# Kernel tuning notes

Hardware: AMD Instinct MI355X
Metric: run time of the kernel (lower is better)

The kernel has to match this reference:

```python
import jax, jax.numpy as jnp
import numpy as np

N_NODES = 100000
N_EDGES = 1600000
DIMS = [512, 200, 175, 125, 75, 50]


def setup_inputs() -> dict:
    key = jax.random.key(0)
    ks = jax.random.split(key, 12)
    inp = {
        "x": jax.random.normal(ks[0], (N_NODES, DIMS[0]), dtype=jnp.float32),
        "edge_index": jax.random.randint(ks[1], (2, N_EDGES), 0, N_NODES, dtype=jnp.int32),
    }
    for i in range(5):
        fan_in, fan_out = DIMS[i], DIMS[i + 1]
        scale = 1.0 / np.sqrt(fan_in)
        inp[f"W{i+1}"] = jax.random.uniform(ks[2 + 2 * i], (fan_in, fan_out), minval=-scale, maxval=scale, dtype=jnp.float32)
        inp[f"b{i+1}"] = jnp.zeros((fan_out,), dtype=jnp.float32)
    return inp


def _gcn_norm(edge_index, n_nodes):
    # add self loops, then symmetric normalization D^-1/2 (A+I) D^-1/2
    loop = jnp.arange(n_nodes, dtype=edge_index.dtype)
    src = jnp.concatenate([edge_index[0], loop])
    dst = jnp.concatenate([edge_index[1], loop])
    deg = jax.ops.segment_sum(jnp.ones_like(dst, dtype=jnp.float32), dst, num_segments=n_nodes)
    dinv = jnp.where(deg > 0, jax.lax.rsqrt(deg), 0.0)
    norm = dinv[src] * dinv[dst]  # [E+N]
    return src, dst, norm


def _gcn_layer(x, W, b, src, dst, norm, n_nodes):
    h = x @ W                                   # [N, out] dense GEMM
    msg = h[src] * norm[:, None]                # gather + scale  [E+N, out]
    agg = jax.ops.segment_sum(msg, dst, num_segments=n_nodes)  # scatter-add
    return agg + b


def reference(x, edge_index, W1, b1, W2, b2, W3, b3, W4, b4, W5, b5):
    n = x.shape[0]
    src, dst, norm = _gcn_norm(edge_index, n)
    h = jax.nn.relu(_gcn_layer(x, W1, b1, src, dst, norm, n))
    h = jax.nn.relu(_gcn_layer(h, W2, b2, src, dst, norm, n))
    h = jax.nn.relu(_gcn_layer(h, W3, b3, src, dst, norm, n))
    h = jax.nn.relu(_gcn_layer(h, W4, b4, src, dst, norm, n))
    return _gcn_layer(h, W5, b5, src, dst, norm, n)
```

## Files before the change

### kernel.cpp

```cpp
#include <hip/hip_runtime.h>
#include <hip/hip_bf16.h>


typedef float f32x4 __attribute__((ext_vector_type(4)));
typedef short bf16x8 __attribute__((ext_vector_type(8)));

static const int GDIMS[6] = {512, 200, 175, 125, 75, 50};
static const int GPAD[6]  = {512, 224, 192, 128, 96, 64};


__global__ void zero_kernel(int* __restrict__ p, int n) {
    int i = blockIdx.x * blockDim.x + threadIdx.x;
    for (; i < n; i += gridDim.x * blockDim.x) p[i] = 0;
}

__global__ void hist_kernel(const int* __restrict__ dst, int E, int* __restrict__ deg) {
    int i = blockIdx.x * blockDim.x + threadIdx.x;
    for (; i < E; i += gridDim.x * blockDim.x) atomicAdd(&deg[dst[i]], 1);
}

__global__ __launch_bounds__(1024) void scan_kernel(const int* __restrict__ deg,
                                                    int* __restrict__ rowptr, int N) {
    __shared__ int sums[1024];
    int t = threadIdx.x;
    int chunk = (N + 1023) >> 10;
    int lo = t * chunk;
    int hi = lo + chunk; if (hi > N) hi = N;
    if (lo > N) lo = N;
    int s = 0;
    for (int i = lo; i < hi; ++i) s += deg[i];
    sums[t] = s;
    __syncthreads();
    for (int off = 1; off < 1024; off <<= 1) {
        int v = (t >= off) ? sums[t - off] : 0;
        __syncthreads();
        sums[t] += v;
        __syncthreads();
    }
    int run = (t > 0) ? sums[t - 1] : 0;
    for (int i = lo; i < hi; ++i) { rowptr[i] = run; run += deg[i]; }
    if (t == 1023) rowptr[N] = run;
}

__global__ void dinv_kernel(const int* __restrict__ deg, float* __restrict__ dinv, int N) {
    int i = blockIdx.x * blockDim.x + threadIdx.x;
    for (; i < N; i += gridDim.x * blockDim.x)
        dinv[i] = rsqrtf((float)(deg[i] + 1));
}

__global__ void copy_kernel(const int* __restrict__ a, int* __restrict__ b, int n) {
    int i = blockIdx.x * blockDim.x + threadIdx.x;
    for (; i < n; i += gridDim.x * blockDim.x) b[i] = a[i];
}

__global__ void scatter_kernel(const int* __restrict__ src, const int* __restrict__ dst,
                               int E, int* __restrict__ cursor, int* __restrict__ csrc) {
    int i = blockIdx.x * blockDim.x + threadIdx.x;
    for (; i < E; i += gridDim.x * blockDim.x) {
        int d = dst[i];
        int pos = atomicAdd(&cursor[d], 1);
        csrc[pos] = src[i];
    }
}


__global__ void wsplit_kernel(const float* __restrict__ W, int K, int Nout,
                              int Kp, ushort* __restrict__ Whi, ushort* __restrict__ Wlo) {
    int k = blockIdx.x * blockDim.x + threadIdx.x;
    int n = blockIdx.y;
    if (k >= Kp) return;
    float v = (k < K && n < Nout) ? W[(size_t)k * Nout + n] : 0.f;
    __bf16 h = (__bf16)v;
    ushort hb = __builtin_bit_cast(ushort, h);
    float hf = __builtin_bit_cast(float, (unsigned)hb << 16);
    __bf16 l = (__bf16)(v - hf);
    Whi[(size_t)n * Kp + k] = hb;
    Wlo[(size_t)n * Kp + k] = __builtin_bit_cast(ushort, l);
}


__device__ inline f32x4 mfma16(bf16x8 a, bf16x8 b, f32x4 c) {
    return __builtin_amdgcn_mfma_f32_16x16x32_bf16(a, b, c, 0, 0, 0);
}

__device__ inline void split8(f32x4 a0, f32x4 a1, bf16x8& hi, bf16x8& lo) {
    float af[8] = {a0[0], a0[1], a0[2], a0[3], a1[0], a1[1], a1[2], a1[3]};
#pragma unroll
    for (int e = 0; e < 8; ++e) {
        __bf16 h = (__bf16)af[e];
        ushort hb = __builtin_bit_cast(ushort, h);
        float hf = __builtin_bit_cast(float, (unsigned)hb << 16);
        __bf16 l = (__bf16)(af[e] - hf);
        hi[e] = (short)hb;
        lo[e] = __builtin_bit_cast(short, l);
    }
}

template<int WM, int WN>
__global__ __launch_bounds__(WM * WN * 64) void gemm_t(
    const float* __restrict__ A, int lda, int Arows,
    const ushort* __restrict__ Bhi, const ushort* __restrict__ Blo, int Kp,
    const float* __restrict__ dinv, int N,
    float* __restrict__ C, int ldc)
{
    constexpr int BM = WM * 64;
    constexpr int T = WM * WN * 64;
    constexpr int SROW = BM + 2;
    __shared__ ushort Ah[4 * SROW * 8];
    __shared__ ushort Al[4 * SROW * 8];

    const int tid = threadIdx.x;
    const int lane = tid & 63;
    const int wave = tid >> 6;
    const int wm = (WM == 1) ? 0 : (wave % WM);
    const int wn = (WM == 1) ? wave : (wave / WM);
    const int m0 = blockIdx.x * BM;
    const int kg = lane >> 4;
    const int l16 = lane & 15;

    const ushort* bp[4];
#pragma unroll
    for (int fn = 0; fn < 4; ++fn) {
        int n = wn * 64 + fn * 16 + l16;
        bp[fn] = Bhi + (size_t)n * Kp + kg * 8;
    }
    const size_t lo_off = (size_t)(Blo - Bhi);

    f32x4 acc[4][4];
#pragma unroll
    for (int i = 0; i < 4; ++i)
#pragma unroll
        for (int j = 0; j < 4; ++j) acc[i][j] = (f32x4)0.f;

    for (int k0 = 0; k0 < Kp; k0 += 32) {
        for (int j = tid; j < BM * 4; j += T) {
            int row = j >> 2, jk = j & 3;
            int gr = m0 + row; if (gr > Arows - 1) gr = Arows - 1;
            const float* ap = A + (size_t)gr * lda + k0 + jk * 8;
            f32x4 a0 = *(const f32x4*)ap;
            f32x4 a1 = *(const f32x4*)(ap + 4);
            bf16x8 hi, lo;
            split8(a0, a1, hi, lo);
            int idx = (jk * SROW + row) * 8;
            *(bf16x8*)&Ah[idx] = hi;
            *(bf16x8*)&Al[idx] = lo;
        }
        __syncthreads();

        bf16x8 bh[4], bl[4], ah[4], al[4];
#pragma unroll
        for (int fn = 0; fn < 4; ++fn) {
            bh[fn] = *(const bf16x8*)(bp[fn] + k0);
            bl[fn] = *(const bf16x8*)(bp[fn] + lo_off + k0);
        }
#pragma unroll
        for (int fm = 0; fm < 4; ++fm) {
            int idx = (kg * SROW + wm * 64 + fm * 16 + l16) * 8;
            ah[fm] = *(const bf16x8*)&Ah[idx];
            al[fm] = *(const bf16x8*)&Al[idx];
        }
#pragma unroll
        for (int fm = 0; fm < 4; ++fm)
#pragma unroll
            for (int fn = 0; fn < 4; ++fn) {
                acc[fm][fn] = mfma16(ah[fm], bh[fn], acc[fm][fn]);
                acc[fm][fn] = mfma16(ah[fm], bl[fn], acc[fm][fn]);
                acc[fm][fn] = mfma16(al[fm], bh[fn], acc[fm][fn]);
            }
        __syncthreads();
    }

    float dv[4][4];
#pragma unroll
    for (int fm = 0; fm < 4; ++fm)
#pragma unroll
        for (int r = 0; r < 4; ++r) {
            int row = m0 + wm * 64 + fm * 16 + kg * 4 + r;
            dv[fm][r] = (row < N) ? dinv[row] : 0.f;
        }
#pragma unroll
    for (int fm = 0; fm < 4; ++fm)
#pragma unroll
        for (int fn = 0; fn < 4; ++fn) {
            int col = wn * 64 + fn * 16 + l16;
            if (col < ldc) {
#pragma unroll
                for (int r = 0; r < 4; ++r) {
                    int row = m0 + wm * 64 + fm * 16 + kg * 4 + r;
                    C[(size_t)row * ldc + col] = acc[fm][fn][r] * dv[fm][r];
                }
            }
        }
}


template<int L>
__global__ __launch_bounds__(256) void agg_t(
    const float* __restrict__ g, int ldg, int nd4,
    const int* __restrict__ rowptr, const int* __restrict__ csrc,
    const float* __restrict__ dinv, const float* __restrict__ bias,
    int D, int N, float* __restrict__ out, int ldo, int relu, int fin)
{
    int node = blockIdx.x * (256 / L) + threadIdx.x / L;
    if (node >= N) return;
    int f4 = threadIdx.x & (L - 1);
    if (f4 >= nd4) return;

    const f32x4* g4 = (const f32x4*)g;
    int ld4 = ldg >> 2;
    f32x4 a0 = g4[(size_t)node * ld4 + f4];
    f32x4 a1 = (f32x4)0.f, a2 = (f32x4)0.f, a3 = (f32x4)0.f;
    int beg = rowptr[node], end = rowptr[node + 1];
    int j = beg;
    for (; j + 3 < end; j += 4) {
        int s0 = csrc[j], s1 = csrc[j + 1], s2 = csrc[j + 2], s3 = csrc[j + 3];
        a0 += g4[(size_t)s0 * ld4 + f4];
        a1 += g4[(size_t)s1 * ld4 + f4];
        a2 += g4[(size_t)s2 * ld4 + f4];
        a3 += g4[(size_t)s3 * ld4 + f4];
    }
    for (; j < end; ++j) a0 += g4[(size_t)csrc[j] * ld4 + f4];

    f32x4 s = (a0 + a1) + (a2 + a3);
    float di = dinv[node];
    if (fin) {
#pragma unroll
        for (int e = 0; e < 4; ++e) {
            int f = f4 * 4 + e;
            if (f < D) out[(size_t)node * ldo + f] = fmaf(di, s[e], bias[f]);
        }
    } else {
        f32x4 v;
#pragma unroll
        for (int e = 0; e < 4; ++e) {
            int f = f4 * 4 + e;
            float val = (f < D) ? fmaf(di, s[e], bias[f]) : 0.f;
            if (relu) val = fmaxf(val, 0.f);
            v[e] = val;
        }
        *(f32x4*)(out + (size_t)node * ldo + f4 * 4) = v;
    }
}


extern "C" void kernel_launch(void* const* d_in, const int* in_sizes, int n_in,
                              void* d_out, int out_size, void* d_ws, size_t ws_size,
                              hipStream_t stream) {
    const float* x = (const float*)d_in[0];
    const int* ei = (const int*)d_in[1];
    int E = in_sizes[1] / 2;
    int N = in_sizes[0] / GDIMS[0];
    int Mp = ((N + 255) / 256) * 256;
    const int* src = ei;
    const int* dst = ei + E;

    const float* W[5];
    const float* bia[5];
    for (int i = 0; i < 5; ++i) {
        W[i] = (const float*)d_in[2 + 2 * i];
        bia[i] = (const float*)d_in[3 + 2 * i];
    }

    char* ws = (char*)d_ws;
    size_t off = 0;
    auto alloc = [&](size_t bytes) -> void* {
        void* p = ws + off;
        off += (bytes + 255) & ~(size_t)255;
        return p;
    };
    int* deg = (int*)alloc((size_t)N * 4);
    int* rowptr = (int*)alloc((size_t)(N + 1) * 4);
    int* cursor = (int*)alloc((size_t)N * 4);
    float* dinv = (float*)alloc((size_t)N * 4);
    int* csrc = (int*)alloc((size_t)E * 4);
    float* buf0 = (float*)alloc((size_t)Mp * 224 * 4);
    float* buf1 = (float*)alloc((size_t)Mp * 224 * 4);
    ushort* Whi[5];
    ushort* Wlo[5];
    int NB[5];
    for (int l = 0; l < 5; ++l) {
        int Kp = GPAD[l];
        NB[l] = ((GPAD[l + 1] + 63) / 64) * 64;
        if (l == 0) NB[l] = 256;
        Whi[l] = (ushort*)alloc((size_t)NB[l] * Kp * 2);
        Wlo[l] = (ushort*)alloc((size_t)NB[l] * Kp * 2);
    }
    (void)ws_size;

    zero_kernel<<<1024, 256, 0, stream>>>(deg, N);
    hist_kernel<<<2048, 256, 0, stream>>>(dst, E, deg);
    scan_kernel<<<1, 1024, 0, stream>>>(deg, rowptr, N);
    dinv_kernel<<<512, 256, 0, stream>>>(deg, dinv, N);
    copy_kernel<<<512, 256, 0, stream>>>(rowptr, cursor, N);
    scatter_kernel<<<2048, 256, 0, stream>>>(src, dst, E, cursor, csrc);

    for (int l = 0; l < 5; ++l) {
        int Kp = GPAD[l];
        dim3 gw((Kp + 255) / 256, NB[l]);
        wsplit_kernel<<<gw, 256, 0, stream>>>(W[l], GDIMS[l], GDIMS[l + 1], Kp,
                                              Whi[l], Wlo[l]);
    }

    for (int l = 0; l < 5; ++l) {
        int Kp = GPAD[l];
        int Pout = GPAD[l + 1];
        int D = GDIMS[l + 1];
        const float* Ain = (l == 0) ? x : buf1;
        int lda = GPAD[l];

        if (l == 0) {
            gemm_t<1, 4><<<Mp / 64, 256, 0, stream>>>(Ain, lda, N, Whi[l], Wlo[l], Kp,
                                                      dinv, N, buf0, Pout);
        } else if (l == 1) {
            gemm_t<1, 3><<<Mp / 64, 192, 0, stream>>>(Ain, lda, N, Whi[l], Wlo[l], Kp,
                                                      dinv, N, buf0, Pout);
        } else if (l == 2 || l == 3) {
            gemm_t<2, 2><<<Mp / 128, 256, 0, stream>>>(Ain, lda, N, Whi[l], Wlo[l], Kp,
                                                       dinv, N, buf0, Pout);
        } else {
            gemm_t<4, 1><<<Mp / 256, 256, 0, stream>>>(Ain, lda, N, Whi[l], Wlo[l], Kp,
                                                       dinv, N, buf0, Pout);
        }

        int nd4 = (D + 3) / 4;
        float* outp = (l == 4) ? (float*)d_out : buf1;
        int ldo = (l == 4) ? D : Pout;
        int relu = (l < 4) ? 1 : 0;
        int fin = (l == 4) ? 1 : 0;
        if (l <= 1) {
            int npb = 256 / 64;
            agg_t<64><<<(N + npb - 1) / npb, 256, 0, stream>>>(buf0, Pout, nd4, rowptr,
                                                               csrc, dinv, bia[l], D, N,
                                                               outp, ldo, relu, fin);
        } else if (l <= 3) {
            int npb = 256 / 32;
            agg_t<32><<<(N + npb - 1) / npb, 256, 0, stream>>>(buf0, Pout, nd4, rowptr,
                                                               csrc, dinv, bia[l], D, N,
                                                               outp, ldo, relu, fin);
        } else {
            int npb = 256 / 16;
            agg_t<16><<<(N + npb - 1) / npb, 256, 0, stream>>>(buf0, Pout, nd4, rowptr,
                                                               csrc, dinv, bia[l], D, N,
                                                               outp, ldo, relu, fin);
        }
    }
    (void)out_size; (void)n_in;
}
```

Baseline: 1.294 ms.

## Emit bf16 hi/lo activations from aggregation and add direct-load bf16 GEMM

The aggregation kernel now writes the next layer's input already split into bf16 hi/lo planes, so layers 2-5 use a new GEMM that loads pre-split operands straight from global memory with no LDS staging or per-tile conversion. Aggregation threads are packed densely per node (only the needed float4 lanes), which removes idle lanes. The gather loop is unrolled to 8 independent accumulators. This trades the LDS-based GEMM for uncached direct global loads and adds an extra write of the split activations.

```diff
diff --git a/kernel.cpp b/kernel.cpp
--- a/kernel.cpp
+++ b/kernel.cpp
@@ -4,6 +4,7 @@
 
 typedef float f32x4 __attribute__((ext_vector_type(4)));
 typedef short bf16x8 __attribute__((ext_vector_type(8)));
+typedef ushort u16x4 __attribute__((ext_vector_type(4)));
 
 static const int GDIMS[6] = {512, 200, 175, 125, 75, 50};
 static const int GPAD[6]  = {512, 224, 192, 128, 96, 64};
@@ -96,8 +97,9 @@
     }
 }
 
+
 template<int WM, int WN>
-__global__ __launch_bounds__(WM * WN * 64) void gemm_t(
+__global__ __launch_bounds__(WM * WN * 64) void gemm_f32(
     const float* __restrict__ A, int lda, int Arows,
     const ushort* __restrict__ Bhi, const ushort* __restrict__ Blo, int Kp,
     const float* __restrict__ dinv, int N,
@@ -170,14 +172,6 @@
         __syncthreads();
     }
 
-    float dv[4][4];
-#pragma unroll
-    for (int fm = 0; fm < 4; ++fm)
-#pragma unroll
-        for (int r = 0; r < 4; ++r) {
-            int row = m0 + wm * 64 + fm * 16 + kg * 4 + r;
-            dv[fm][r] = (row < N) ? dinv[row] : 0.f;
-        }
 #pragma unroll
     for (int fm = 0; fm < 4; ++fm)
 #pragma unroll
@@ -187,58 +181,159 @@
 #pragma unroll
                 for (int r = 0; r < 4; ++r) {
                     int row = m0 + wm * 64 + fm * 16 + kg * 4 + r;
-                    C[(size_t)row * ldc + col] = acc[fm][fn][r] * dv[fm][r];
+                    float dv = (row < N) ? dinv[row] : 0.f;
+                    C[(size_t)row * ldc + col] = acc[fm][fn][r] * dv;
                 }
             }
         }
 }
 
 
-template<int L>
+template<int WM, int WN>
+__global__ __launch_bounds__(WM * WN * 64) void gemm_bf(
+    const ushort* __restrict__ Ahi, const ushort* __restrict__ Alo, int lda, int Arows,
+    const ushort* __restrict__ Bhi, const ushort* __restrict__ Blo, int Kp,
+    const float* __restrict__ dinv, int N,
+    float* __restrict__ C, int ldc)
+{
+    const int lane = threadIdx.x & 63;
+    const int wave = threadIdx.x >> 6;
+    const int wm = (WM == 1) ? 0 : (wave % WM);
+    const int wn = (WM == 1) ? wave : (wave / WM);
+    const int m0 = blockIdx.x * (WM * 64);
+    const int kg = lane >> 4;
+    const int l16 = lane & 15;
+
+    const ushort* ap[4];
+#pragma unroll
+    for (int fm = 0; fm < 4; ++fm) {
+        int row = m0 + wm * 64 + fm * 16 + l16;
+        if (row > Arows - 1) row = Arows - 1;
+        ap[fm] = Ahi + (size_t)row * lda + kg * 8;
+    }
+    const size_t alo = (size_t)(Alo - Ahi);
+    const ushort* bp[4];
+#pragma unroll
+    for (int fn = 0; fn < 4; ++fn) {
+        int n = wn * 64 + fn * 16 + l16;
+        bp[fn] = Bhi + (size_t)n * Kp + kg * 8;
+    }
+    const size_t blo = (size_t)(Blo - Bhi);
+
+    f32x4 acc[4][4];
+#pragma unroll
+    for (int i = 0; i < 4; ++i)
+#pragma unroll
+        for (int j = 0; j < 4; ++j) acc[i][j] = (f32x4)0.f;
+
+    for (int k0 = 0; k0 < Kp; k0 += 32) {
+        bf16x8 ah[4], al4[4], bh[4], bl[4];
+#pragma unroll
+        for (int fm = 0; fm < 4; ++fm) {
+            ah[fm] = *(const bf16x8*)(ap[fm] + k0);
+            al4[fm] = *(const bf16x8*)(ap[fm] + alo + k0);
+        }
+#pragma unroll
+        for (int fn = 0; fn < 4; ++fn) {
+            bh[fn] = *(const bf16x8*)(bp[fn] + k0);
+            bl[fn] = *(const bf16x8*)(bp[fn] + blo + k0);
+        }
+#pragma unroll
+        for (int fm = 0; fm < 4; ++fm)
+#pragma unroll
+            for (int fn = 0; fn < 4; ++fn) {
+                acc[fm][fn] = mfma16(ah[fm], bh[fn], acc[fm][fn]);
+                acc[fm][fn] = mfma16(ah[fm], bl[fn], acc[fm][fn]);
+                acc[fm][fn] = mfma16(al4[fm], bh[fn], acc[fm][fn]);
+            }
+    }
+
+#pragma unroll
+    for (int fm = 0; fm < 4; ++fm)
+#pragma unroll
+        for (int fn = 0; fn < 4; ++fn) {
+            int col = wn * 64 + fn * 16 + l16;
+            if (col < ldc) {
+#pragma unroll
+                for (int r = 0; r < 4; ++r) {
+                    int row = m0 + wm * 64 + fm * 16 + kg * 4 + r;
+                    float dv = (row < N) ? dinv[row] : 0.f;
+                    C[(size_t)row * ldc + col] = acc[fm][fn][r] * dv;
+                }
+            }
+        }
+}
+
+
+template<int ND4T, bool FIN>
 __global__ __launch_bounds__(256) void agg_t(
-    const float* __restrict__ g, int ldg, int nd4,
+    const float* __restrict__ g, int ld4,
     const int* __restrict__ rowptr, const int* __restrict__ csrc,
     const float* __restrict__ dinv, const float* __restrict__ bias,
-    int D, int N, float* __restrict__ out, int ldo, int relu, int fin)
+    int D, int N,
+    ushort* __restrict__ Ahi, ushort* __restrict__ Alo, int ldo,
+    float* __restrict__ outF, int ldof)
 {
-    int node = blockIdx.x * (256 / L) + threadIdx.x / L;
-    if (node >= N) return;
-    int f4 = threadIdx.x & (L - 1);
-    if (f4 >= nd4) return;
+    unsigned gt = blockIdx.x * 256u + threadIdx.x;
+    unsigned node = gt / (unsigned)ND4T;
+    unsigned f4 = gt - node * (unsigned)ND4T;
+    if (node >= (unsigned)N) return;
 
     const f32x4* g4 = (const f32x4*)g;
-    int ld4 = ldg >> 2;
-    f32x4 a0 = g4[(size_t)node * ld4 + f4];
+    const unsigned l4 = (unsigned)ld4;
+
+    f32x4 a0 = g4[(size_t)node * l4 + f4];
     f32x4 a1 = (f32x4)0.f, a2 = (f32x4)0.f, a3 = (f32x4)0.f;
+    f32x4 a4 = (f32x4)0.f, a5 = (f32x4)0.f, a6 = (f32x4)0.f, a7 = (f32x4)0.f;
+
     int beg = rowptr[node], end = rowptr[node + 1];
     int j = beg;
+    for (; j + 7 < end; j += 8) {
+        unsigned s0 = csrc[j],     s1 = csrc[j + 1], s2 = csrc[j + 2], s3 = csrc[j + 3];
+        unsigned s4 = csrc[j + 4], s5 = csrc[j + 5], s6 = csrc[j + 6], s7 = csrc[j + 7];
+        a0 += g4[(size_t)s0 * l4 + f4];
+        a1 += g4[(size_t)s1 * l4 + f4];
+        a2 += g4[(size_t)s2 * l4 + f4];
+        a3 += g4[(size_t)s3 * l4 + f4];
+        a4 += g4[(size_t)s4 * l4 + f4];
+        a5 += g4[(size_t)s5 * l4 + f4];
+        a6 += g4[(size_t)s6 * l4 + f4];
+        a7 += g4[(size_t)s7 * l4 + f4];
+    }
     for (; j + 3 < end; j += 4) {
-        int s0 = csrc[j], s1 = csrc[j + 1], s2 = csrc[j + 2], s3 = csrc[j + 3];
-        a0 += g4[(size_t)s0 * ld4 + f4];
-        a1 += g4[(size_t)s1 * ld4 + f4];
-        a2 += g4[(size_t)s2 * ld4 + f4];
-        a3 += g4[(size_t)s3 * ld4 + f4];
-    }
-    for (; j < end; ++j) a0 += g4[(size_t)csrc[j] * ld4 + f4];
-
-    f32x4 s = (a0 + a1) + (a2 + a3);
+        unsigned s0 = csrc[j], s1 = csrc[j + 1], s2 = csrc[j + 2], s3 = csrc[j + 3];
+        a0 += g4[(size_t)s0 * l4 + f4];
+        a1 += g4[(size_t)s1 * l4 + f4];
+        a2 += g4[(size_t)s2 * l4 + f4];
+        a3 += g4[(size_t)s3 * l4 + f4];
+    }
+    for (; j < end; ++j) a0 += g4[(size_t)csrc[j] * l4 + f4];
+
+    f32x4 s = ((a0 + a1) + (a2 + a3)) + ((a4 + a5) + (a6 + a7));
     float di = dinv[node];
-    if (fin) {
+
+    if (FIN) {
 #pragma unroll
         for (int e = 0; e < 4; ++e) {
-            int f = f4 * 4 + e;
-            if (f < D) out[(size_t)node * ldo + f] = fmaf(di, s[e], bias[f]);
+            int f = (int)f4 * 4 + e;
+            if (f < D) outF[(size_t)node * ldof + f] = fmaf(di, s[e], bias[f]);
         }
     } else {
-        f32x4 v;
+        u16x4 hv, lv;
 #pragma unroll
         for (int e = 0; e < 4; ++e) {
-            int f = f4 * 4 + e;
-            float val = (f < D) ? fmaf(di, s[e], bias[f]) : 0.f;
-            if (relu) val = fmaxf(val, 0.f);
-            v[e] = val;
-        }
-        *(f32x4*)(out + (size_t)node * ldo + f4 * 4) = v;
+            int f = (int)f4 * 4 + e;
+            float val = 0.f;
+            if (f < D) val = fmaxf(fmaf(di, s[e], bias[f]), 0.f);
+            __bf16 h = (__bf16)val;
+            ushort hb = __builtin_bit_cast(ushort, h);
+            float hf = __builtin_bit_cast(float, (unsigned)hb << 16);
+            __bf16 l = (__bf16)(val - hf);
+            hv[e] = hb;
+            lv[e] = __builtin_bit_cast(ushort, l);
+        }
+        *(u16x4*)(Ahi + (size_t)node * ldo + f4 * 4) = hv;
+        *(u16x4*)(Alo + (size_t)node * ldo + f4 * 4) = lv;
     }
 }
 
@@ -273,15 +368,14 @@
     int* cursor = (int*)alloc((size_t)N * 4);
     float* dinv = (float*)alloc((size_t)N * 4);
     int* csrc = (int*)alloc((size_t)E * 4);
-    float* buf0 = (float*)alloc((size_t)Mp * 224 * 4);
-    float* buf1 = (float*)alloc((size_t)Mp * 224 * 4);
+    float* g = (float*)alloc((size_t)Mp * 224 * 4);
+    ushort* Ahi = (ushort*)alloc((size_t)Mp * 224 * 2);
+    ushort* Alo = (ushort*)alloc((size_t)Mp * 224 * 2);
     ushort* Whi[5];
     ushort* Wlo[5];
-    int NB[5];
+    int NB[5] = {256, 192, 128, 128, 64};
     for (int l = 0; l < 5; ++l) {
         int Kp = GPAD[l];
-        NB[l] = ((GPAD[l + 1] + 63) / 64) * 64;
-        if (l == 0) NB[l] = 256;
         Whi[l] = (ushort*)alloc((size_t)NB[l] * Kp * 2);
         Wlo[l] = (ushort*)alloc((size_t)NB[l] * Kp * 2);
     }
@@ -301,48 +395,32 @@
                                               Whi[l], Wlo[l]);
     }
 
-    for (int l = 0; l < 5; ++l) {
-        int Kp = GPAD[l];
-        int Pout = GPAD[l + 1];
-        int D = GDIMS[l + 1];
-        const float* Ain = (l == 0) ? x : buf1;
-        int lda = GPAD[l];
-
-        if (l == 0) {
-            gemm_t<1, 4><<<Mp / 64, 256, 0, stream>>>(Ain, lda, N, Whi[l], Wlo[l], Kp,
-                                                      dinv, N, buf0, Pout);
-        } else if (l == 1) {
-            gemm_t<1, 3><<<Mp / 64, 192, 0, stream>>>(Ain, lda, N, Whi[l], Wlo[l], Kp,
-                                                      dinv, N, buf0, Pout);
-        } else if (l == 2 || l == 3) {
-            gemm_t<2, 2><<<Mp / 128, 256, 0, stream>>>(Ain, lda, N, Whi[l], Wlo[l], Kp,
-                                                       dinv, N, buf0, Pout);
-        } else {
-            gemm_t<4, 1><<<Mp / 256, 256, 0, stream>>>(Ain, lda, N, Whi[l], Wlo[l], Kp,
-                                                       dinv, N, buf0, Pout);
-        }
-
-        int nd4 = (D + 3) / 4;
-        float* outp = (l == 4) ? (float*)d_out : buf1;
-        int ldo = (l == 4) ? D : Pout;
-        int relu = (l < 4) ? 1 : 0;
-        int fin = (l == 4) ? 1 : 0;
-        if (l <= 1) {
-            int npb = 256 / 64;
-            agg_t<64><<<(N + npb - 1) / npb, 256, 0, stream>>>(buf0, Pout, nd4, rowptr,
-                                                               csrc, dinv, bia[l], D, N,
-                                                               outp, ldo, relu, fin);
-        } else if (l <= 3) {
-            int npb = 256 / 32;
-            agg_t<32><<<(N + npb - 1) / npb, 256, 0, stream>>>(buf0, Pout, nd4, rowptr,
-                                                               csrc, dinv, bia[l], D, N,
-                                                               outp, ldo, relu, fin);
-        } else {
-            int npb = 256 / 16;
-            agg_t<16><<<(N + npb - 1) / npb, 256, 0, stream>>>(buf0, Pout, nd4, rowptr,
-                                                               csrc, dinv, bia[l], D, N,
-                                                               outp, ldo, relu, fin);
-        }
-    }
+    auto aggBlocks = [&](int nd4t) { return ((size_t)N * nd4t + 255) / 256; };
+
+    gemm_f32<1, 4><<<Mp / 64, 256, 0, stream>>>(x, 512, N, Whi[0], Wlo[0], 512,
+                                                dinv, N, g, 224);
+    agg_t<56, false><<<aggBlocks(56), 256, 0, stream>>>(g, 56, rowptr, csrc, dinv,
+                                                        bia[0], 200, N, Ahi, Alo, 224,
+                                                        nullptr, 0);
+    gemm_bf<1, 3><<<Mp / 64, 192, 0, stream>>>(Ahi, Alo, 224, N, Whi[1], Wlo[1], 224,
+                                               dinv, N, g, 192);
+    agg_t<48, false><<<aggBlocks(48), 256, 0, stream>>>(g, 48, rowptr, csrc, dinv,
+                                                        bia[1], 175, N, Ahi, Alo, 192,
+                                                        nullptr, 0);
+    gemm_bf<2, 2><<<Mp / 128, 256, 0, stream>>>(Ahi, Alo, 192, N, Whi[2], Wlo[2], 192,
+                                                dinv, N, g, 128);
+    agg_t<32, false><<<aggBlocks(32), 256, 0, stream>>>(g, 32, rowptr, csrc, dinv,
+                                                        bia[2], 125, N, Ahi, Alo, 128,
+                                                        nullptr, 0);
+    gemm_bf<2, 2><<<Mp / 128, 256, 0, stream>>>(Ahi, Alo, 128, N, Whi[3], Wlo[3], 128,
+                                                dinv, N, g, 96);
+    agg_t<24, false><<<aggBlocks(24), 256, 0, stream>>>(g, 24, rowptr, csrc, dinv,
+                                                        bia[3], 75, N, Ahi, Alo, 96,
+                                                        nullptr, 0);
+    gemm_bf<4, 1><<<Mp / 256, 256, 0, stream>>>(Ahi, Alo, 96, N, Whi[4], Wlo[4], 96,
+                                                dinv, N, g, 64);
+    agg_t<13, true><<<aggBlocks(13), 256, 0, stream>>>(g, 16, rowptr, csrc, dinv,
+                                                       bia[4], 50, N, nullptr, nullptr, 0,
+                                                       (float*)d_out, 50);
     (void)out_size; (void)n_in;
 }
```

Result: slower. 1.419 ms (+9.7%).

## Add double-buffered GEMM with register prefetch for the first two layers

Applied to the files above, without the earlier changes.

Adds a gemm_d kernel that processes K in 64-wide steps with two LDS buffers. The next A tile is loaded into registers before the current MFMAs and split into bf16 hi/lo parts after them, so there is one barrier per step instead of two per 32-wide step. Layers 1 and 2, which have the largest K, use it, and the layer loop is unrolled into explicit launches. The cost is more registers and twice the shared memory, which may reduce occupancy.

```diff
diff --git a/kernel.cpp b/kernel.cpp
--- a/kernel.cpp
+++ b/kernel.cpp
@@ -4,9 +4,9 @@
 
 typedef float f32x4 __attribute__((ext_vector_type(4)));
 typedef short bf16x8 __attribute__((ext_vector_type(8)));
+typedef ushort u16x8 __attribute__((ext_vector_type(8)));
 
 static const int GDIMS[6] = {512, 200, 175, 125, 75, 50};
-static const int GPAD[6]  = {512, 224, 192, 128, 96, 64};
 
 
 __global__ void zero_kernel(int* __restrict__ p, int n) {
@@ -83,7 +83,7 @@
     return __builtin_amdgcn_mfma_f32_16x16x32_bf16(a, b, c, 0, 0, 0);
 }
 
-__device__ inline void split8(f32x4 a0, f32x4 a1, bf16x8& hi, bf16x8& lo) {
+__device__ inline void split8(f32x4 a0, f32x4 a1, u16x8& hi, u16x8& lo) {
     float af[8] = {a0[0], a0[1], a0[2], a0[3], a1[0], a1[1], a1[2], a1[3]};
 #pragma unroll
     for (int e = 0; e < 8; ++e) {
@@ -91,10 +91,146 @@
         ushort hb = __builtin_bit_cast(ushort, h);
         float hf = __builtin_bit_cast(float, (unsigned)hb << 16);
         __bf16 l = (__bf16)(af[e] - hf);
-        hi[e] = (short)hb;
-        lo[e] = __builtin_bit_cast(short, l);
-    }
-}
+        hi[e] = hb;
+        lo[e] = __builtin_bit_cast(ushort, l);
+    }
+}
+
+
+template<int WM, int WN>
+__global__ __launch_bounds__(WM * WN * 64) void gemm_d(
+    const float* __restrict__ A, int lda, int Arows,
+    const ushort* __restrict__ Bhi, const ushort* __restrict__ Blo, int Kp,
+    const float* __restrict__ dinv, int N,
+    float* __restrict__ C, int ldc)
+{
+    constexpr int BM = WM * 64;
+    constexpr int T = WM * WN * 64;
+    constexpr int SROW = BM + 2;
+    constexpr int NCH = BM * 8;
+    constexpr int PT = (NCH + T - 1) / T;
+    constexpr int BUFS = 8 * SROW * 8;
+    __shared__ ushort Ah[2 * BUFS];
+    __shared__ ushort Al[2 * BUFS];
+
+    const int tid = threadIdx.x;
+    const int lane = tid & 63;
+    const int wave = tid >> 6;
+    const int wm = (WM == 1) ? 0 : (wave % WM);
+    const int wn = (WM == 1) ? wave : (wave / WM);
+    const int m0 = blockIdx.x * BM;
+    const int kg = lane >> 4;
+    const int l16 = lane & 15;
+
+    const ushort* bp[4];
+#pragma unroll
+    for (int fn = 0; fn < 4; ++fn)
+        bp[fn] = Bhi + (size_t)(wn * 64 + fn * 16 + l16) * Kp + kg * 8;
+    const size_t blo = (size_t)(Blo - Bhi);
+
+    f32x4 acc[4][4];
+#pragma unroll
+    for (int i = 0; i < 4; ++i)
+#pragma unroll
+        for (int j = 0; j < 4; ++j) acc[i][j] = (f32x4)0.f;
+
+    const float* cap[PT];
+    int cidx[PT], ckk[PT];
+    bool cok[PT];
+#pragma unroll
+    for (int p = 0; p < PT; ++p) {
+        int j = tid + p * T;
+        cok[p] = j < NCH;
+        int row = cok[p] ? (j >> 3) : 0;
+        int jkq = cok[p] ? (j & 7) : 0;
+        int gr = m0 + row; if (gr > Arows - 1) gr = Arows - 1;
+        cap[p] = A + (size_t)gr * lda + jkq * 8;
+        cidx[p] = (jkq * SROW + row) * 8;
+        ckk[p] = jkq * 8;
+    }
+
+#pragma unroll
+    for (int p = 0; p < PT; ++p) {
+        if (cok[p]) {
+            f32x4 a0 = *(const f32x4*)(cap[p]);
+            f32x4 a1 = *(const f32x4*)(cap[p] + 4);
+            u16x8 hi, lo;
+            split8(a0, a1, hi, lo);
+            *(u16x8*)&Ah[cidx[p]] = hi;
+            *(u16x8*)&Al[cidx[p]] = lo;
+        }
+    }
+    __syncthreads();
+
+    const int nIter = (Kp + 63) >> 6;
+    f32x4 ra0[PT], ra1[PT];
+    for (int it = 0; it < nIter; ++it) {
+        const int buf = (it & 1) * BUFS;
+        const int kbase = it << 6;
+        const int nkb = kbase + 64;
+        const bool hasNext = nkb < Kp;
+        if (hasNext) {
+#pragma unroll
+            for (int p = 0; p < PT; ++p)
+                if (cok[p] && nkb + ckk[p] < Kp) {
+                    ra0[p] = *(const f32x4*)(cap[p] + nkb);
+                    ra1[p] = *(const f32x4*)(cap[p] + nkb + 4);
+                }
+        }
+#pragma unroll
+        for (int s = 0; s < 2; ++s) {
+            if (kbase + s * 32 >= Kp) break;
+            bf16x8 ah[4], al4[4], bh[4], bl[4];
+#pragma unroll
+            for (int fn = 0; fn < 4; ++fn) {
+                bh[fn] = *(const bf16x8*)(bp[fn] + kbase + s * 32);
+                bl[fn] = *(const bf16x8*)(bp[fn] + blo + kbase + s * 32);
+            }
+#pragma unroll
+            for (int fm = 0; fm < 4; ++fm) {
+                int idx = buf + ((s * 4 + kg) * SROW + wm * 64 + fm * 16 + l16) * 8;
+                ah[fm] = *(const bf16x8*)&Ah[idx];
+                al4[fm] = *(const bf16x8*)&Al[idx];
+            }
+#pragma unroll
+            for (int fm = 0; fm < 4; ++fm)
+#pragma unroll
+                for (int fn = 0; fn < 4; ++fn) {
+                    acc[fm][fn] = mfma16(ah[fm], bh[fn], acc[fm][fn]);
+                    acc[fm][fn] = mfma16(ah[fm], bl[fn], acc[fm][fn]);
+                    acc[fm][fn] = mfma16(al4[fm], bh[fn], acc[fm][fn]);
+                }
+        }
+        if (hasNext) {
+            const int obuf = buf ^ BUFS;
+#pragma unroll
+            for (int p = 0; p < PT; ++p)
+                if (cok[p] && nkb + ckk[p] < Kp) {
+                    u16x8 hi, lo;
+                    split8(ra0[p], ra1[p], hi, lo);
+                    *(u16x8*)&Ah[obuf + cidx[p]] = hi;
+                    *(u16x8*)&Al[obuf + cidx[p]] = lo;
+                }
+        }
+        __syncthreads();
+    }
+
+#pragma unroll
+    for (int fm = 0; fm < 4; ++fm)
+#pragma unroll
+        for (int fn = 0; fn < 4; ++fn) {
+            int col = wn * 64 + fn * 16 + l16;
+            if (col < ldc) {
+#pragma unroll
+                for (int r = 0; r < 4; ++r) {
+                    int row = m0 + wm * 64 + fm * 16 + kg * 4 + r;
+                    float dv = (row < N) ? dinv[row] : 0.f;
+                    C[(size_t)row * ldc + col] = acc[fm][fn][r] * dv;
+                }
+            }
+        }
+}
+
 
 template<int WM, int WN>
 __global__ __launch_bounds__(WM * WN * 64) void gemm_t(
@@ -139,14 +275,13 @@
             const float* ap = A + (size_t)gr * lda + k0 + jk * 8;
             f32x4 a0 = *(const f32x4*)ap;
             f32x4 a1 = *(const f32x4*)(ap + 4);
-            bf16x8 hi, lo;
+            u16x8 hi, lo;
             split8(a0, a1, hi, lo);
             int idx = (jk * SROW + row) * 8;
-            *(bf16x8*)&Ah[idx] = hi;
-            *(bf16x8*)&Al[idx] = lo;
+            *(u16x8*)&Ah[idx] = hi;
+            *(u16x8*)&Al[idx] = lo;
         }
         __syncthreads();
-
         bf16x8 bh[4], bl[4], ah[4], al[4];
 #pragma unroll
         for (int fn = 0; fn < 4; ++fn) {
@@ -170,14 +305,6 @@
         __syncthreads();
     }
 
-    float dv[4][4];
-#pragma unroll
-    for (int fm = 0; fm < 4; ++fm)
-#pragma unroll
-        for (int r = 0; r < 4; ++r) {
-            int row = m0 + wm * 64 + fm * 16 + kg * 4 + r;
-            dv[fm][r] = (row < N) ? dinv[row] : 0.f;
-        }
 #pragma unroll
     for (int fm = 0; fm < 4; ++fm)
 #pragma unroll
@@ -187,7 +314,8 @@
 #pragma unroll
                 for (int r = 0; r < 4; ++r) {
                     int row = m0 + wm * 64 + fm * 16 + kg * 4 + r;
-                    C[(size_t)row * ldc + col] = acc[fm][fn][r] * dv[fm][r];
+                    float dv = (row < N) ? dinv[row] : 0.f;
+                    C[(size_t)row * ldc + col] = acc[fm][fn][r] * dv;
                 }
             }
         }
@@ -273,17 +401,15 @@
     int* cursor = (int*)alloc((size_t)N * 4);
     float* dinv = (float*)alloc((size_t)N * 4);
     int* csrc = (int*)alloc((size_t)E * 4);
-    float* buf0 = (float*)alloc((size_t)Mp * 224 * 4);
+    float* g = (float*)alloc((size_t)Mp * 224 * 4);
     float* buf1 = (float*)alloc((size_t)Mp * 224 * 4);
     ushort* Whi[5];
     ushort* Wlo[5];
-    int NB[5];
+    int NB[5] = {256, 192, 128, 128, 64};
+    int KP[5] = {512, 224, 192, 128, 96};
     for (int l = 0; l < 5; ++l) {
-        int Kp = GPAD[l];
-        NB[l] = ((GPAD[l + 1] + 63) / 64) * 64;
-        if (l == 0) NB[l] = 256;
-        Whi[l] = (ushort*)alloc((size_t)NB[l] * Kp * 2);
-        Wlo[l] = (ushort*)alloc((size_t)NB[l] * Kp * 2);
+        Whi[l] = (ushort*)alloc((size_t)NB[l] * KP[l] * 2);
+        Wlo[l] = (ushort*)alloc((size_t)NB[l] * KP[l] * 2);
     }
     (void)ws_size;
 
@@ -295,54 +421,30 @@
     scatter_kernel<<<2048, 256, 0, stream>>>(src, dst, E, cursor, csrc);
 
     for (int l = 0; l < 5; ++l) {
-        int Kp = GPAD[l];
-        dim3 gw((Kp + 255) / 256, NB[l]);
-        wsplit_kernel<<<gw, 256, 0, stream>>>(W[l], GDIMS[l], GDIMS[l + 1], Kp,
+        dim3 gw((KP[l] + 255) / 256, NB[l]);
+        wsplit_kernel<<<gw, 256, 0, stream>>>(W[l], GDIMS[l], GDIMS[l + 1], KP[l],
                                               Whi[l], Wlo[l]);
     }
 
-    for (int l = 0; l < 5; ++l) {
-        int Kp = GPAD[l];
-        int Pout = GPAD[l + 1];
-        int D = GDIMS[l + 1];
-        const float* Ain = (l == 0) ? x : buf1;
-        int lda = GPAD[l];
-
-        if (l == 0) {
-            gemm_t<1, 4><<<Mp / 64, 256, 0, stream>>>(Ain, lda, N, Whi[l], Wlo[l], Kp,
-                                                      dinv, N, buf0, Pout);
-        } else if (l == 1) {
-            gemm_t<1, 3><<<Mp / 64, 192, 0, stream>>>(Ain, lda, N, Whi[l], Wlo[l], Kp,
-                                                      dinv, N, buf0, Pout);
-        } else if (l == 2 || l == 3) {
-            gemm_t<2, 2><<<Mp / 128, 256, 0, stream>>>(Ain, lda, N, Whi[l], Wlo[l], Kp,
-                                                       dinv, N, buf0, Pout);
-        } else {
-            gemm_t<4, 1><<<Mp / 256, 256, 0, stream>>>(Ain, lda, N, Whi[l], Wlo[l], Kp,
-                                                       dinv, N, buf0, Pout);
-        }
-
-        int nd4 = (D + 3) / 4;
-        float* outp = (l == 4) ? (float*)d_out : buf1;
-        int ldo = (l == 4) ? D : Pout;
-        int relu = (l < 4) ? 1 : 0;
-        int fin = (l == 4) ? 1 : 0;
-        if (l <= 1) {
-            int npb = 256 / 64;
-            agg_t<64><<<(N + npb - 1) / npb, 256, 0, stream>>>(buf0, Pout, nd4, rowptr,
-                                                               csrc, dinv, bia[l], D, N,
-                                                               outp, ldo, relu, fin);
-        } else if (l <= 3) {
-            int npb = 256 / 32;
-            agg_t<32><<<(N + npb - 1) / npb, 256, 0, stream>>>(buf0, Pout, nd4, rowptr,
-                                                               csrc, dinv, bia[l], D, N,
-                                                               outp, ldo, relu, fin);
-        } else {
-            int npb = 256 / 16;
-            agg_t<16><<<(N + npb - 1) / npb, 256, 0, stream>>>(buf0, Pout, nd4, rowptr,
-                                                               csrc, dinv, bia[l], D, N,
-                                                               outp, ldo, relu, fin);
-        }
-    }
+    gemm_d<1, 4><<<Mp / 64, 256, 0, stream>>>(x, 512, N, Whi[0], Wlo[0], 512,
+                                              dinv, N, g, 224);
+    agg_t<64><<<(N + 3) / 4, 256, 0, stream>>>(g, 224, 50, rowptr, csrc, dinv,
+                                               bia[0], 200, N, buf1, 224, 1, 0);
+    gemm_d<1, 3><<<Mp / 64, 192, 0, stream>>>(buf1, 224, N, Whi[1], Wlo[1], 224,
+                                              dinv, N, g, 192);
+    agg_t<64><<<(N + 3) / 4, 256, 0, stream>>>(g, 192, 44, rowptr, csrc, dinv,
+                                               bia[1], 175, N, buf1, 192, 1, 0);
+    gemm_t<2, 2><<<Mp / 128, 256, 0, stream>>>(buf1, 192, N, Whi[2], Wlo[2], 192,
+                                               dinv, N, g, 128);
+    agg_t<32><<<(N + 7) / 8, 256, 0, stream>>>(g, 128, 32, rowptr, csrc, dinv,
+                                               bia[2], 125, N, buf1, 128, 1, 0);
+    gemm_t<2, 2><<<Mp / 128, 256, 0, stream>>>(buf1, 128, N, Whi[3], Wlo[3], 128,
+                                               dinv, N, g, 96);
+    agg_t<32><<<(N + 7) / 8, 256, 0, stream>>>(g, 96, 19, rowptr, csrc, dinv,
+                                               bia[3], 75, N, buf1, 96, 1, 0);
+    gemm_t<4, 1><<<Mp / 256, 256, 0, stream>>>(buf1, 96, N, Whi[4], Wlo[4], 96,
+                                               dinv, N, g, 64);
+    agg_t<16><<<(N + 15) / 16, 256, 0, stream>>>(g, 64, 13, rowptr, csrc, dinv,
+                                                 bia[4], 50, N, (float*)d_out, 50, 0, 1);
     (void)out_size; (void)n_in;
 }
```

Measured after the change: 1.427 ms. 10.3% more time.
